# Kernel tuning notes

Measured on AMD Instinct MI355X. Metric: run time of the kernel, lower is better.

## Reference

```python
import jax, jax.numpy as jnp
import numpy as np

N_TYPES = 3
PER_TYPE = 333333
N = N_TYPES * PER_TYPE
F = 64       # feats_dim per node type
H = 64       # hidden_dim
OUT = 64     # out_dim
D1 = 100     # distinct degrees (count)
D2 = 100     # distinct degrees (count2)
T = 50000    # number of target nodes


def leaky(x):
    # nn.LeakyReLU(negative_slope=0.7)
    return jnp.where(x >= 0, x, 0.7 * x)


def setup_inputs() -> dict:
    key = jax.random.key(0)
    ks = jax.random.split(key, 12)
    s = 0.05
    return {
        "f0": jax.random.normal(ks[0], (PER_TYPE, F), jnp.float32),
        "f1": jax.random.normal(ks[1], (PER_TYPE, F), jnp.float32),
        "f2": jax.random.normal(ks[2], (PER_TYPE, F), jnp.float32),
        "W": jax.random.normal(ks[3], (N_TYPES, F, H), jnp.float32) * s,
        "b": jnp.zeros((N_TYPES, H), jnp.float32),
        "Wc": jax.random.normal(ks[4], (N_TYPES, D1 + D2, H), jnp.float32) * s,
        "bc": jnp.zeros((N_TYPES, H), jnp.float32),
        "Wout": jax.random.normal(ks[5], (2 * H, OUT), jnp.float32) * s,
        "bout": jnp.zeros((OUT,), jnp.float32),
        "type_mask": jnp.repeat(jnp.arange(N_TYPES, dtype=jnp.int32), PER_TYPE),
        "degree_index": jax.random.randint(ks[6], (N,), 0, D1, jnp.int32),
        "degree_index2": jax.random.randint(ks[7], (N,), 0, D2, jnp.int32),
        "target_node_indices": jax.random.randint(ks[8], (T,), 0, N, jnp.int32),
    }


def reference(f0, f1, f2, W, b, Wc, bc, Wout, bout,
              type_mask, degree_index, degree_index2, target_node_indices):
    n = type_mask.shape[0]
    # degree one-hot embeddings: eye[degree_index] concat eye[degree_index2] -> [N, D1+D2]
    deg = jnp.concatenate([
        jax.nn.one_hot(degree_index, D1, dtype=jnp.float32),
        jax.nn.one_hot(degree_index2, D2, dtype=jnp.float32),
    ], axis=1)

    feats = (f0, f1, f2)
    tf = jnp.zeros((n, H), jnp.float32)
    tfc = jnp.zeros((n, H), jnp.float32)
    for i in range(N_TYPES):
        idx = jnp.nonzero(type_mask == i, size=PER_TYPE)[0]   # gather indices for type i
        h_i = leaky(feats[i] @ W[i] + b[i])                   # [P, H]
        tf = tf.at[idx].set(h_i)                              # scatter into pre-zeroed buffer
        hc_i = leaky(deg[idx] @ Wc[i] + bc[i])                # gather degree rows -> [P, H]
        tfc = tfc.at[idx].set(hc_i)

    # concat, (dropout rate 0 => identity), cast to half as in original
    x = jnp.concatenate([tf, tfc], axis=1).astype(jnp.float16)  # [N, 2H]
    h = x  # ctr_ntype_layer placeholder (identity; source class unavailable)
    logits = h @ Wout.astype(jnp.float16) + bout.astype(jnp.float16)  # [N, OUT]
    return logits[target_node_indices], h[target_node_indices]
```

## Files before the change

### kernel.cpp

```cpp
#include <hip/hip_runtime.h>
#include <hip/hip_fp16.h>

typedef _Float16 half8 __attribute__((ext_vector_type(8)));
typedef _Float16 half2v __attribute__((ext_vector_type(2)));
typedef float f32x2 __attribute__((ext_vector_type(2)));
typedef float f32x4 __attribute__((ext_vector_type(4)));

__device__ __forceinline__ float leakyf(float v) { return v >= 0.f ? v : 0.7f * v; }

__global__ __launch_bounds__(512, 4)
void shgnn_fused2(const float* __restrict__ f0, const float* __restrict__ f1,
                  const float* __restrict__ f2, const float* __restrict__ W,
                  const float* __restrict__ b, const float* __restrict__ Wc,
                  const float* __restrict__ bc, const float* __restrict__ Wout,
                  const float* __restrict__ bout,
                  const int* __restrict__ tgt, const int* __restrict__ deg1,
                  const int* __restrict__ deg2,
                  int T, int per_type,
                  float* __restrict__ out_logits, float* __restrict__ out_h)
{
    __shared__ _Float16 sWF[24 * 512];
    __shared__ _Float16 sOF[16 * 512];
    __shared__ _Float16 sX[8][2048];
    __shared__ float sB[192];
    __shared__ float sBC[192];
    __shared__ float sBout[64];

    const int tid = threadIdx.x;

    for (int i = tid; i < 3 * 64 * 64; i += 512) {
        const int K = i >> 6, col = i & 63;
        const int ks = K >> 5, j = K & 7;
        const int ln = (((K >> 3) & 3) << 4) | (col & 15);
        const int n = col >> 4;
        sWF[((ks * 4 + n) << 9) + (ln << 3) + j] = (_Float16)W[i];
    }
    for (int i = tid; i < 128 * 64; i += 512) {
        const int k = i >> 6, col = i & 63;
        const int ks = k >> 5, j = k & 7;
        const int ln = (((k >> 3) & 3) << 4) | (col & 15);
        const int n = col >> 4;
        sOF[((ks * 4 + n) << 9) + (ln << 3) + j] = (_Float16)Wout[i];
    }
    if (tid < 192) sB[tid] = b[tid];
    if (tid < 192) sBC[tid] = bc[tid];
    if (tid < 64)  sBout[tid] = bout[tid];
    __syncthreads();

    const int lane = tid & 63;
    const int l15 = lane & 15;
    const int lq  = lane >> 4;
    char* const sXw = (char*)sX[tid >> 6];

    const int ntiles = (T + 15) >> 4;
    const int gwave = blockIdx.x * 8 + (tid >> 6);
    const int nwaves = gridDim.x * 8;

    for (int tile = gwave; tile < ntiles; tile += nwaves) {
        int t = tile * 16 + l15;
        if (t >= T) t = T - 1;
        const int nnv = tgt[t];
        const int tyv = (nnv >= 2 * per_type) ? 2 : (nnv >= per_type ? 1 : 0);

        #pragma unroll
        for (int r = 0; r < 16; ++r) {
            const int nr = __builtin_amdgcn_readlane(nnv, r);
            const int tyr = (nr >= 2 * per_type) ? 2 : (nr >= per_type ? 1 : 0);
            const float* fbr = (tyr == 0) ? f0 : ((tyr == 1) ? f1 : f2);
            const float fv = fbr[(size_t)(nr - tyr * per_type) * 64 + lane];
            const int d1r = deg1[nr];
            const int d2r = deg2[nr];
            const float* wcb = Wc + (size_t)tyr * 12800;
            const float h2 = leakyf(wcb[d1r * 64 + lane] + wcb[(100 + d2r) * 64 + lane]
                                    + sBC[tyr * 64 + lane]);
            const int swr = (r & 7) << 4;
            *(_Float16*)(sXw + ((r * 256 + lane * 2) ^ swr))       = (_Float16)fv;
            *(_Float16*)(sXw + ((r * 256 + 128 + lane * 2) ^ swr)) = (_Float16)h2;
        }

        const int swl = (l15 & 7) << 4;
        const half8 a0 = *(const half8*)(sXw + ((l15 * 256 + lq * 16) ^ swl));
        const half8 a1 = *(const half8*)(sXw + ((l15 * 256 + 64 + lq * 16) ^ swl));
        const half8 z8 = {(_Float16)0.f, (_Float16)0.f, (_Float16)0.f, (_Float16)0.f,
                          (_Float16)0.f, (_Float16)0.f, (_Float16)0.f, (_Float16)0.f};
        const int k0 = 2 * tyv, k1 = 2 * tyv + 1;

        int tyr4[4];
        #pragma unroll
        for (int r = 0; r < 4; ++r) tyr4[r] = __shfl(tyv, (lq << 2) + r);

        #pragma unroll
        for (int n = 0; n < 4; ++n) {
            f32x4 acc = {0.f, 0.f, 0.f, 0.f};
            #pragma unroll
            for (int ks = 0; ks < 6; ++ks) {
                const half8 av = (ks == k0) ? a0 : ((ks == k1) ? a1 : z8);
                const half8 wb = *(const half8*)(sWF + ((ks * 4 + n) << 9) + lane * 8);
                acc = __builtin_amdgcn_mfma_f32_16x16x32_f16(av, wb, acc, 0, 0, 0);
            }
            #pragma unroll
            for (int r = 0; r < 4; ++r) {
                const int row = (lq << 2) + r;
                const float v = leakyf(acc[r] + sB[tyr4[r] * 64 + n * 16 + l15]);
                const int off = (row * 256 + (n * 16 + l15) * 2) ^ ((row & 7) << 4);
                *(_Float16*)(sXw + off) = (_Float16)v;
            }
        }

        half8 xa[4];
        #pragma unroll
        for (int ks = 0; ks < 4; ++ks)
            xa[ks] = *(const half8*)(sXw + ((l15 * 256 + ks * 64 + lq * 16) ^ swl));

        #pragma unroll
        for (int n = 0; n < 4; ++n) {
            const float bo = (float)(_Float16)sBout[n * 16 + l15];
            f32x4 acc = {bo, bo, bo, bo};
            #pragma unroll
            for (int ks = 0; ks < 4; ++ks) {
                const half8 wf = *(const half8*)(sOF + ((ks * 4 + n) << 9) + lane * 8);
                acc = __builtin_amdgcn_mfma_f32_16x16x32_f16(xa[ks], wf, acc, 0, 0, 0);
            }
            #pragma unroll
            for (int r = 0; r < 4; ++r) {
                int trr = tile * 16 + (lq << 2) + r;
                if (trr >= T) trr = T - 1;
                out_logits[(size_t)trr * 64 + n * 16 + l15] = (float)(_Float16)acc[r];
            }
        }

        #pragma unroll
        for (int r = 0; r < 16; ++r) {
            int tb = tile * 16 + r;
            if (tb >= T) tb = T - 1;
            const half2v hv = *(const half2v*)(sXw + ((r * 256 + lane * 4) ^ ((r & 7) << 4)));
            f32x2 o = {(float)hv.x, (float)hv.y};
            *(f32x2*)(out_h + (size_t)tb * 128 + lane * 2) = o;
        }
    }
}

extern "C" void kernel_launch(void* const* d_in, const int* in_sizes, int n_in,
                              void* d_out, int out_size, void* d_ws, size_t ws_size,
                              hipStream_t stream) {
    const float* f0   = (const float*)d_in[0];
    const float* f1   = (const float*)d_in[1];
    const float* f2   = (const float*)d_in[2];
    const float* W    = (const float*)d_in[3];
    const float* b    = (const float*)d_in[4];
    const float* Wc   = (const float*)d_in[5];
    const float* bc   = (const float*)d_in[6];
    const float* Wout = (const float*)d_in[7];
    const float* bout = (const float*)d_in[8];
    const int* deg1   = (const int*)d_in[10];
    const int* deg2   = (const int*)d_in[11];
    const int* tgt    = (const int*)d_in[12];

    const int T = in_sizes[12];
    const int per_type = in_sizes[0] / 64;

    float* out_logits = (float*)d_out;
    float* out_h = out_logits + (size_t)T * 64;

    const int ntiles = (T + 15) / 16;
    int blocks = (ntiles + 7) / 8;
    if (blocks > 512) blocks = 512;

    shgnn_fused2<<<dim3(blocks), dim3(512), 0, stream>>>(
        f0, f1, f2, W, b, Wc, bc, Wout, bout,
        tgt, deg1, deg2, T, per_type, out_logits, out_h);
}
```

Before: 23.94 us.

## Prefetch target indices, batch degree gathers, and use nontemporal loads/stores

Target indices for the next tile are prefetched one iteration ahead, and the first load is issued before the weight staging so it overlaps that setup. Degree index loads are batched 8 rows at a time to raise memory-level parallelism. Feature reads and output writes use nontemporal hints to avoid polluting cache, bias values are hoisted into registers, and tiles are interleaved across blocks with a grid of up to 512 blocks. This adds register pressure, and the launch-bound occupancy may suffer.

```diff
diff --git a/kernel.cpp b/kernel.cpp
--- a/kernel.cpp
+++ b/kernel.cpp
@@ -9,7 +9,7 @@
 __device__ __forceinline__ float leakyf(float v) { return v >= 0.f ? v : 0.7f * v; }
 
 __global__ __launch_bounds__(512, 4)
-void shgnn_fused2(const float* __restrict__ f0, const float* __restrict__ f1,
+void shgnn_fused3(const float* __restrict__ f0, const float* __restrict__ f1,
                   const float* __restrict__ f2, const float* __restrict__ W,
                   const float* __restrict__ b, const float* __restrict__ Wc,
                   const float* __restrict__ bc, const float* __restrict__ Wout,
@@ -27,6 +27,22 @@
     __shared__ float sBout[64];
 
     const int tid = threadIdx.x;
+    const int lane = tid & 63;
+    const int l15 = lane & 15;
+    const int lq  = lane >> 4;
+    const int wid = tid >> 6;
+    char* const sXw = (char*)sX[wid];
+
+    const int ntiles = (T + 15) >> 4;
+    const int gwave = blockIdx.x + gridDim.x * wid;
+    const int nwaves = gridDim.x * 8;
+
+    int tile = gwave;
+    int nnv_pre = 0;
+    if (tile < ntiles) {
+        int t = tile * 16 + l15; if (t >= T) t = T - 1;
+        nnv_pre = __builtin_nontemporal_load(tgt + t);
+    }
 
     for (int i = tid; i < 3 * 64 * 64; i += 512) {
         const int K = i >> 6, col = i & 63;
@@ -47,35 +63,42 @@
     if (tid < 64)  sBout[tid] = bout[tid];
     __syncthreads();
 
-    const int lane = tid & 63;
-    const int l15 = lane & 15;
-    const int lq  = lane >> 4;
-    char* const sXw = (char*)sX[tid >> 6];
+    const float bc0 = sBC[lane], bc1 = sBC[64 + lane], bc2 = sBC[128 + lane];
 
-    const int ntiles = (T + 15) >> 4;
-    const int gwave = blockIdx.x * 8 + (tid >> 6);
-    const int nwaves = gridDim.x * 8;
-
-    for (int tile = gwave; tile < ntiles; tile += nwaves) {
-        int t = tile * 16 + l15;
-        if (t >= T) t = T - 1;
-        const int nnv = tgt[t];
+    for (; tile < ntiles; tile += nwaves) {
+        const int nnv = nnv_pre;
+        {
+            const int tn = tile + nwaves;
+            if (tn < ntiles) {
+                int t2 = tn * 16 + l15; if (t2 >= T) t2 = T - 1;
+                nnv_pre = __builtin_nontemporal_load(tgt + t2);
+            }
+        }
         const int tyv = (nnv >= 2 * per_type) ? 2 : (nnv >= per_type ? 1 : 0);
 
         #pragma unroll
-        for (int r = 0; r < 16; ++r) {
-            const int nr = __builtin_amdgcn_readlane(nnv, r);
-            const int tyr = (nr >= 2 * per_type) ? 2 : (nr >= per_type ? 1 : 0);
-            const float* fbr = (tyr == 0) ? f0 : ((tyr == 1) ? f1 : f2);
-            const float fv = fbr[(size_t)(nr - tyr * per_type) * 64 + lane];
-            const int d1r = deg1[nr];
-            const int d2r = deg2[nr];
-            const float* wcb = Wc + (size_t)tyr * 12800;
-            const float h2 = leakyf(wcb[d1r * 64 + lane] + wcb[(100 + d2r) * 64 + lane]
-                                    + sBC[tyr * 64 + lane]);
-            const int swr = (r & 7) << 4;
-            *(_Float16*)(sXw + ((r * 256 + lane * 2) ^ swr))       = (_Float16)fv;
-            *(_Float16*)(sXw + ((r * 256 + 128 + lane * 2) ^ swr)) = (_Float16)h2;
+        for (int h = 0; h < 2; ++h) {
+            int nr[8], d1r[8], d2r[8];
+            #pragma unroll
+            for (int r = 0; r < 8; ++r)
+                nr[r] = __builtin_amdgcn_readlane(nnv, h * 8 + r);
+            #pragma unroll
+            for (int r = 0; r < 8; ++r) { d1r[r] = deg1[nr[r]]; d2r[r] = deg2[nr[r]]; }
+            #pragma unroll
+            for (int r = 0; r < 8; ++r) {
+                const int row = h * 8 + r;
+                const int tyr = (nr[r] >= 2 * per_type) ? 2 : (nr[r] >= per_type ? 1 : 0);
+                const float* fbr = (tyr == 0) ? f0 : ((tyr == 1) ? f1 : f2);
+                const float fv = __builtin_nontemporal_load(
+                    fbr + (size_t)(nr[r] - tyr * per_type) * 64 + lane);
+                const float* wcb = Wc + (size_t)tyr * 12800;
+                const float bcv = (tyr == 0) ? bc0 : ((tyr == 1) ? bc1 : bc2);
+                const float h2 = leakyf(wcb[d1r[r] * 64 + lane]
+                                      + wcb[(100 + d2r[r]) * 64 + lane] + bcv);
+                const int swr = (row & 7) << 4;
+                *(_Float16*)(sXw + ((row * 256 + lane * 2) ^ swr))       = (_Float16)fv;
+                *(_Float16*)(sXw + ((row * 256 + 128 + lane * 2) ^ swr)) = (_Float16)h2;
+            }
         }
 
         const int swl = (l15 & 7) << 4;
@@ -125,7 +148,8 @@
             for (int r = 0; r < 4; ++r) {
                 int trr = tile * 16 + (lq << 2) + r;
                 if (trr >= T) trr = T - 1;
-                out_logits[(size_t)trr * 64 + n * 16 + l15] = (float)(_Float16)acc[r];
+                __builtin_nontemporal_store((float)(_Float16)acc[r],
+                    out_logits + (size_t)trr * 64 + n * 16 + l15);
             }
         }
 
@@ -135,7 +159,7 @@
             if (tb >= T) tb = T - 1;
             const half2v hv = *(const half2v*)(sXw + ((r * 256 + lane * 4) ^ ((r & 7) << 4)));
             f32x2 o = {(float)hv.x, (float)hv.y};
-            *(f32x2*)(out_h + (size_t)tb * 128 + lane * 2) = o;
+            __builtin_nontemporal_store(o, (f32x2*)(out_h + (size_t)tb * 128 + lane * 2));
         }
     }
 }
@@ -163,10 +187,10 @@
     float* out_h = out_logits + (size_t)T * 64;
 
     const int ntiles = (T + 15) / 16;
-    int blocks = (ntiles + 7) / 8;
-    if (blocks > 512) blocks = 512;
+    int blocks = 512;
+    if (ntiles < blocks) blocks = ntiles;
 
-    shgnn_fused2<<<dim3(blocks), dim3(512), 0, stream>>>(
+    shgnn_fused3<<<dim3(blocks), dim3(512), 0, stream>>>(
         f0, f1, f2, W, b, Wc, bc, Wout, bout,
         tgt, deg1, deg2, T, per_type, out_logits, out_h);
 }
```

Measured after the change: 29.67 us. 23.9% more time.
